# Kernel tuning notes

Hardware: AMD Instinct MI355X
Metric: run time of the kernel (lower is better)

The kernel has to match this reference:

```python
import jax, jax.numpy as jnp
import numpy as np

B, L1, L2, H = 16, 2048, 2048, 768


def setup_inputs() -> dict:
    key = jax.random.key(0)
    k1, k2, k3 = jax.random.split(key, 3)
    hi1 = jax.random.normal(k1, (B, L1, H), dtype=jnp.float32)
    hi2 = jax.random.normal(k2, (B, L2, H), dtype=jnp.float32)
    # xavier_uniform: bound = sqrt(6/(H+H))
    bound = float(np.sqrt(6.0 / (H + H)))
    wg = jax.random.uniform(k3, (H, H), dtype=jnp.float32, minval=-bound, maxval=bound)
    return {"hi1": hi1, "hi2": hi2, "wg": wg}


def reference(hi1, hi2, wg):
    # G = (hi1 @ wg) @ hi2^T  -> [B, L1, L2]
    g = jnp.einsum('bik,kl->bil', hi1, wg)
    scores = jnp.einsum('bil,bjl->bij', g, hi2)
    attn = jax.nn.softmax(scores, axis=2)
    # weighted sum over hi2 -> [B, L1, H]
    return jnp.einsum('bij,bjh->bih', attn, hi2)
```

## Files before the change

### kernel.cpp

```cpp
#include <hip/hip_runtime.h>
#include <hip/hip_bf16.h>

#define BB  16
#define LL1 2048
#define LL2 2048
#define HH  768
#define NT  24

typedef __attribute__((ext_vector_type(4))) float f32x4;
typedef __attribute__((ext_vector_type(8))) _Float16 f16x8;
typedef __attribute__((ext_vector_type(4))) _Float16 f16x4;

typedef __attribute__((address_space(3))) unsigned int lds_uint;
typedef __attribute__((address_space(1))) const unsigned int glob_uint;
__device__ __forceinline__ void gl_lds16(const void* g, void* l) {
  __builtin_amdgcn_global_load_lds((glob_uint*)g, (lds_uint*)l, 16, 0, 0);
}

__global__ __launch_bounds__(256) void k_split16(
    const float* __restrict__ in, _Float16* __restrict__ p, int n4)
{
  int i = blockIdx.x * 256 + threadIdx.x;
  int stride = gridDim.x * 256;
  for (; i < n4; i += stride) {
    f32x4 v = ((const f32x4*)in)[i];
    f16x4 o;
#pragma unroll
    for (int q = 0; q < 4; ++q) o[q] = (_Float16)v[q];
    ((f16x4*)p)[i] = o;
  }
}

__global__ __launch_bounds__(256) void k_split_wt16(
    const float* __restrict__ wg, _Float16* __restrict__ wt)
{
  __shared__ float t[32][33];
  const int k0 = blockIdx.y * 32, n0 = blockIdx.x * 32;
  const int tx = threadIdx.x & 31, ty = threadIdx.x >> 5;
#pragma unroll
  for (int r = ty; r < 32; r += 8) t[r][tx] = wg[(size_t)(k0 + r) * HH + n0 + tx];
  __syncthreads();
#pragma unroll
  for (int r = ty; r < 32; r += 8)
    wt[(size_t)(n0 + r) * HH + k0 + tx] = (_Float16)t[tx][r];
}


#define STAGE_SETUP()                                                      \
  size_t goA0, goA1, goB0; int loA0, loA1, loB0;                           \
  {                                                                        \
    int f0 = tid, f1 = 512 + tid;                                          \
    int r0 = f0 >> 2, s0 = f0 & 3, r1 = f1 >> 2, s1 = f1 & 3;              \
    goA0 = (size_t)r0 * HH + (size_t)((s0 ^ (r0 & 3)) * 8);                \
    goA1 = (size_t)r1 * HH + (size_t)((s1 ^ (r1 & 3)) * 8);                \
    loA0 = f0 * 16; loA1 = f1 * 16;                                        \
    int rb = tid >> 2, sb = tid & 3;                                       \
    goB0 = (size_t)rb * HH + (size_t)((sb ^ (rb & 3)) * 8);                \
    loB0 = tid * 16;                                                       \
  }                                                                        \
  int offA[4], offB[4];                                                    \
  _Pragma("unroll")                                                        \
  for (int mi = 0; mi < 4; ++mi) {                                         \
    int r = wm + mi * 16 + fr;                                             \
    offA[mi] = r * 64 + ((l4 * 16) ^ ((r & 3) << 4));                      \
  }                                                                        \
  _Pragma("unroll")                                                        \
  for (int ni = 0; ni < 4; ++ni) {                                         \
    int r = wn + ni * 16 + fr;                                             \
    offB[ni] = r * 64 + ((l4 * 16) ^ ((r & 3) << 4));                      \
  }

#define STG(buf, k0)                                                       \
  gl_lds16(pA + goA0 + (k0), (char*)&sA[buf][0] + loA0);                   \
  gl_lds16(pA + goA1 + (k0), (char*)&sA[buf][0] + loA1);                   \
  gl_lds16(pB + goB0 + (k0), (char*)&sB[buf][0] + loB0);

#define CMP(buf)                                                           \
  {                                                                        \
    f16x8 fa[4], fb[4];                                                    \
    _Pragma("unroll") for (int mi = 0; mi < 4; ++mi)                       \
      fa[mi] = *(const f16x8*)((const char*)&sA[buf][0] + offA[mi]);       \
    _Pragma("unroll") for (int ni = 0; ni < 4; ++ni)                       \
      fb[ni] = *(const f16x8*)((const char*)&sB[buf][0] + offB[ni]);       \
    _Pragma("unroll") for (int mi = 0; mi < 4; ++mi)                       \
      _Pragma("unroll") for (int ni = 0; ni < 4; ++ni)                     \
        acc[mi][ni] = __builtin_amdgcn_mfma_f32_16x16x32_f16(              \
            fa[mi], fb[ni], acc[mi][ni], 0, 0, 0);                         \
  }

#define KLOOP()                                                            \
  STG(0, 0);                                                               \
  asm volatile("s_waitcnt vmcnt(0)" ::: "memory");                         \
  __builtin_amdgcn_s_barrier();                                            \
  __builtin_amdgcn_sched_barrier(0);                                       \
  _Pragma("unroll")                                                        \
  for (int t = 0; t < NT; ++t) {                                           \
    if (t < NT - 1) { STG((t + 1) & 1, (t + 1) * 32); }                    \
    CMP(t & 1);                                                            \
    asm volatile("s_waitcnt vmcnt(0)" ::: "memory");                       \
    __builtin_amdgcn_s_barrier();                                          \
    __builtin_amdgcn_sched_barrier(0);                                     \
  }

__global__ __launch_bounds__(512, 4) void k_gemm_f16(
    const _Float16* __restrict__ A, const _Float16* __restrict__ Bt,
    _Float16* __restrict__ C)
{
  __shared__ _Float16 sA[2][256 * 32], sB[2][128 * 32];
  const int tid = threadIdx.x, lane = tid & 63, wave = tid >> 6;
  const int wm = (wave >> 1) * 64, wn = (wave & 1) * 64;
  const int m0 = blockIdx.y * 256, n0 = blockIdx.x * 128;
  const int fr = lane & 15, l4 = lane >> 4;
  const _Float16* pA = A  + (size_t)m0 * HH;
  const _Float16* pB = Bt + (size_t)n0 * HH;
  f32x4 acc[4][4] = {};
  STAGE_SETUP();
  KLOOP();

#pragma unroll
  for (int mi = 0; mi < 4; ++mi)
#pragma unroll
    for (int ni = 0; ni < 4; ++ni)
#pragma unroll
      for (int j = 0; j < 4; ++j) {
        int row = m0 + wm + mi * 16 + (lane >> 4) * 4 + j;
        int col = n0 + wn + ni * 16 + fr;
        C[(size_t)row * HH + col] = (_Float16)acc[mi][ni][j];
      }
}

__global__ __launch_bounds__(512, 4) void k_scores_f16(
    const _Float16* __restrict__ G, const _Float16* __restrict__ H2,
    _Float16* __restrict__ S16, float* __restrict__ Mx, int b_base)
{
  __shared__ _Float16 sA[2][256 * 32], sB[2][128 * 32];
  const int tid = threadIdx.x, lane = tid & 63, wave = tid >> 6;
  const int wm = (wave >> 1) * 64, wn = (wave & 1) * 64;
  const int z = blockIdx.z, b = b_base + z;
  const int i0 = blockIdx.y * 256, j0 = blockIdx.x * 128;
  const int fr = lane & 15, l4 = lane >> 4;
  const _Float16* pA = G  + (size_t)b * LL1 * HH + (size_t)i0 * HH;
  const _Float16* pB = H2 + (size_t)b * LL2 * HH + (size_t)j0 * HH;
  _Float16* Sp = S16 + (size_t)z * LL1 * LL2;
  float* Mp = Mx + (size_t)z * LL1 * 16;
  f32x4 acc[4][4] = {};
  STAGE_SETUP();
  KLOOP();

  __syncthreads();
  float* smax = (float*)&sA[0][0];
#pragma unroll
  for (int mi = 0; mi < 4; ++mi)
#pragma unroll
    for (int j = 0; j < 4; ++j) {
      float rm = fmaxf(fmaxf(acc[mi][0][j], acc[mi][1][j]),
                       fmaxf(acc[mi][2][j], acc[mi][3][j]));
#pragma unroll
      for (int off = 8; off >= 1; off >>= 1) rm = fmaxf(rm, __shfl_xor(rm, off));
      if ((lane & 15) == 0)
        smax[(wm + mi * 16 + (lane >> 4) * 4 + j) * 2 + (wave & 1)] = rm;
    }
  __syncthreads();

#pragma unroll
  for (int mi = 0; mi < 4; ++mi)
#pragma unroll
    for (int j = 0; j < 4; ++j) {
      int rloc = wm + mi * 16 + (lane >> 4) * 4 + j;
      float tmax = fmaxf(smax[rloc * 2], smax[rloc * 2 + 1]);
      int row = i0 + rloc;
#pragma unroll
      for (int ni = 0; ni < 4; ++ni) {
        int col = j0 + wn + ni * 16 + fr;
        float d = fmaxf(acc[mi][ni][j] - tmax, -28.0f);
        Sp[(size_t)row * LL2 + col] = (_Float16)d;
      }
    }
  if (tid < 256)
    Mp[(size_t)(i0 + tid) * 16 + (j0 >> 7)] = fmaxf(smax[tid * 2], smax[tid * 2 + 1]);
}

__global__ __launch_bounds__(512) void k_select(
    const _Float16* __restrict__ S16, const float* __restrict__ Mx,
    const _Float16* __restrict__ H2f, float* __restrict__ Out, int b_base)
{
  const int tid = threadIdx.x, lane = tid & 63, wv = tid >> 6;
  const int z = blockIdx.y, b = b_base + z;
  const int row = blockIdx.x * 4 + (wv >> 1);
  const int half = wv & 1;
  const _Float16* srow = S16 + ((size_t)z * LL1 + row) * LL2;
  const _Float16* V = H2f + (size_t)b * LL2 * HH;

  float bmax = Mx[((size_t)z * LL1 + row) * 16 + (lane & 15)];
  float m = bmax;
#pragma unroll
  for (int off = 8; off >= 1; off >>= 1) m = fmaxf(m, __shfl_xor(m, off));

  const float thr = m - 20.0f;
  float acc[6] = {};
  float lsum = 0.f;

  for (int jb = 0; jb < 16; ++jb) {
    float bj = __shfl(bmax, jb);
    if (bj <= thr) continue;
#pragma unroll
    for (int h = 0; h < 2; ++h) {
      float sval = bj + (float)srow[jb * 128 + h * 64 + lane];
      bool hit = sval > thr;
      unsigned long long mask = __ballot(hit);
      float p = hit ? __expf(sval - m) : 0.f;
      lsum += p;
      while (mask) {
        int src = __ffsll((long long)mask) - 1;
        mask &= mask - 1;
        float w = __shfl(p, src);
        int j = jb * 128 + h * 64 + src;
        const _Float16* vr = V + (size_t)j * HH + half * 384;
#pragma unroll
        for (int c = 0; c < 6; ++c) acc[c] = fmaf(w, (float)vr[lane + 64 * c], acc[c]);
      }
    }
  }
#pragma unroll
  for (int off = 32; off >= 1; off >>= 1) lsum += __shfl_xor(lsum, off);
  const float inv = 1.0f / lsum;
  float* orow = Out + ((size_t)b * LL1 + row) * HH + half * 384;
#pragma unroll
  for (int c = 0; c < 6; ++c) orow[lane + 64 * c] = acc[c] * inv;
}

extern "C" void kernel_launch(void* const* d_in, const int* in_sizes, int n_in,
                              void* d_out, int out_size, void* d_ws, size_t ws_size,
                              hipStream_t stream) {
  const float* hi1 = (const float*)d_in[0];
  const float* hi2 = (const float*)d_in[1];
  const float* wg  = (const float*)d_in[2];
  float* out = (float*)d_out;

  char* ws = (char*)d_ws;
  const size_t plane_elems = (size_t)BB * LL1 * HH;
  const size_t plane_b = plane_elems * 2;
  const size_t wt_b = (size_t)HH * HH * 2;
  const size_t s16_per_b = (size_t)LL1 * LL2 * 2;
  const size_t m_per_b = (size_t)LL1 * 16 * 4;

  _Float16* H2f = (_Float16*)ws;
  _Float16* Gf  = (_Float16*)(ws + plane_b);
  _Float16* Wtf = (_Float16*)(ws + 2 * plane_b);
  char* X = ws + 2 * plane_b + wt_b;
  _Float16* H1f = (_Float16*)X;

  const size_t fixed = 2 * plane_b + wt_b;
  int CB = 1;
  const int cand[5] = {16, 8, 4, 2, 1};
  for (int i = 0; i < 5; ++i) {
    size_t xneed = (size_t)cand[i] * (s16_per_b + m_per_b);
    if (xneed < plane_b) xneed = plane_b;
    if (fixed + xneed + 1024 <= ws_size) { CB = cand[i]; break; }
  }
  _Float16* S16 = (_Float16*)X;
  float* Mbuf = (float*)(X + (size_t)CB * s16_per_b);

  k_split16<<<4096, 256, 0, stream>>>(hi1, H1f, (int)(plane_elems / 4));
  k_split16<<<4096, 256, 0, stream>>>(hi2, H2f, (int)(plane_elems / 4));
  k_split_wt16<<<dim3(HH / 32, HH / 32), 256, 0, stream>>>(wg, Wtf);

  k_gemm_f16<<<dim3(HH / 128, (BB * LL1) / 256), 512, 0, stream>>>(H1f, Wtf, Gf);

  for (int b0 = 0; b0 < BB; b0 += CB) {
    k_scores_f16<<<dim3(LL2 / 128, LL1 / 256, CB), 512, 0, stream>>>(Gf, H2f, S16, Mbuf, b0);
    k_select<<<dim3(LL1 / 4, CB), 512, 0, stream>>>(S16, Mbuf, H2f, out, b0);
  }
}
```

Measured before the change: 400.4 us.

## Enlarge GEMM tiles to 256x256 with 64-wide K steps and split-phase prefetch

Both MFMA GEMM kernels move from 256x128 to 256x256 block tiles. Each wave now holds an 8x4 accumulator grid over a 128x64 subtile, and the K step grows to 64, split into two 32-wide LDS phases that are prefetched separately with partial vmcnt waits. The LDS swizzle changes to xor on (row>>1)&3, and s_setprio raises wave priority around the MFMA bursts. The scores kernel's row-max epilogue is adjusted to four column waves and writes two per-128-column max entries. The goal is more data reuse per LDS byte and fewer barriers per FLOP, at the cost of more registers and LDS per block and lower occupancy (launch bounds drop to 2 blocks per SM).

```diff
diff --git a/kernel.cpp b/kernel.cpp
--- a/kernel.cpp
+++ b/kernel.cpp
@@ -5,7 +5,7 @@
 #define LL1 2048
 #define LL2 2048
 #define HH  768
-#define NT  24
+#define NKT 12
 
 typedef __attribute__((ext_vector_type(4))) float f32x4;
 typedef __attribute__((ext_vector_type(8))) _Float16 f16x8;
@@ -46,138 +46,152 @@
 }
 
 
-#define STAGE_SETUP()                                                      \
-  size_t goA0, goA1, goB0; int loA0, loA1, loB0;                           \
-  {                                                                        \
-    int f0 = tid, f1 = 512 + tid;                                          \
-    int r0 = f0 >> 2, s0 = f0 & 3, r1 = f1 >> 2, s1 = f1 & 3;              \
-    goA0 = (size_t)r0 * HH + (size_t)((s0 ^ (r0 & 3)) * 8);                \
-    goA1 = (size_t)r1 * HH + (size_t)((s1 ^ (r1 & 3)) * 8);                \
-    loA0 = f0 * 16; loA1 = f1 * 16;                                        \
-    int rb = tid >> 2, sb = tid & 3;                                       \
-    goB0 = (size_t)rb * HH + (size_t)((sb ^ (rb & 3)) * 8);                \
-    loB0 = tid * 16;                                                       \
-  }                                                                        \
-  int offA[4], offB[4];                                                    \
-  _Pragma("unroll")                                                        \
-  for (int mi = 0; mi < 4; ++mi) {                                         \
-    int r = wm + mi * 16 + fr;                                             \
-    offA[mi] = r * 64 + ((l4 * 16) ^ ((r & 3) << 4));                      \
-  }                                                                        \
-  _Pragma("unroll")                                                        \
-  for (int ni = 0; ni < 4; ++ni) {                                         \
-    int r = wn + ni * 16 + fr;                                             \
-    offB[ni] = r * 64 + ((l4 * 16) ^ ((r & 3) << 4));                      \
-  }
-
-#define STG(buf, k0)                                                       \
-  gl_lds16(pA + goA0 + (k0), (char*)&sA[buf][0] + loA0);                   \
-  gl_lds16(pA + goA1 + (k0), (char*)&sA[buf][0] + loA1);                   \
-  gl_lds16(pB + goB0 + (k0), (char*)&sB[buf][0] + loB0);
-
-#define CMP(buf)                                                           \
-  {                                                                        \
-    f16x8 fa[4], fb[4];                                                    \
-    _Pragma("unroll") for (int mi = 0; mi < 4; ++mi)                       \
-      fa[mi] = *(const f16x8*)((const char*)&sA[buf][0] + offA[mi]);       \
-    _Pragma("unroll") for (int ni = 0; ni < 4; ++ni)                       \
-      fb[ni] = *(const f16x8*)((const char*)&sB[buf][0] + offB[ni]);       \
-    _Pragma("unroll") for (int mi = 0; mi < 4; ++mi)                       \
-      _Pragma("unroll") for (int ni = 0; ni < 4; ++ni)                     \
-        acc[mi][ni] = __builtin_amdgcn_mfma_f32_16x16x32_f16(              \
-            fa[mi], fb[ni], acc[mi][ni], 0, 0, 0);                         \
-  }
-
-#define KLOOP()                                                            \
-  STG(0, 0);                                                               \
-  asm volatile("s_waitcnt vmcnt(0)" ::: "memory");                         \
-  __builtin_amdgcn_s_barrier();                                            \
-  __builtin_amdgcn_sched_barrier(0);                                       \
-  _Pragma("unroll")                                                        \
-  for (int t = 0; t < NT; ++t) {                                           \
-    if (t < NT - 1) { STG((t + 1) & 1, (t + 1) * 32); }                    \
-    CMP(t & 1);                                                            \
-    asm volatile("s_waitcnt vmcnt(0)" ::: "memory");                       \
-    __builtin_amdgcn_s_barrier();                                          \
-    __builtin_amdgcn_sched_barrier(0);                                     \
-  }
-
-__global__ __launch_bounds__(512, 4) void k_gemm_f16(
+#define STAGE_SETUP()                                                       \
+  size_t gA0, gA1; int lA0, lA1;                                            \
+  {                                                                         \
+    int f0 = tid, f1 = 512 + tid;                                           \
+    int r0 = f0 >> 2, s0 = f0 & 3, r1 = f1 >> 2, s1 = f1 & 3;               \
+    gA0 = (size_t)r0 * HH + (size_t)((s0 ^ ((r0 >> 1) & 3)) * 8);           \
+    gA1 = (size_t)r1 * HH + (size_t)((s1 ^ ((r1 >> 1) & 3)) * 8);           \
+    lA0 = f0 * 16; lA1 = f1 * 16;                                           \
+  }                                                                         \
+  int offA[8], offB[4];                                                     \
+  _Pragma("unroll")                                                         \
+  for (int mi = 0; mi < 8; ++mi) {                                          \
+    int r = wml + mi * 16 + fr;                                             \
+    offA[mi] = r * 64 + ((l4 ^ ((r >> 1) & 3)) * 16);                       \
+  }                                                                         \
+  _Pragma("unroll")                                                         \
+  for (int ni = 0; ni < 4; ++ni) {                                          \
+    int r = wnl + ni * 16 + fr;                                             \
+    offB[ni] = r * 64 + ((l4 ^ ((r >> 1) & 3)) * 16);                       \
+  }
+
+#define STG_A(db, kk, kt)                                                   \
+  gl_lds16(pA + gA0 + (kt) * 64 + (kk) * 32, (char*)&sA[db][kk][0] + lA0);  \
+  gl_lds16(pA + gA1 + (kt) * 64 + (kk) * 32, (char*)&sA[db][kk][0] + lA1);
+#define STG_B(db, kk, kt)                                                   \
+  gl_lds16(pB + gA0 + (kt) * 64 + (kk) * 32, (char*)&sB[db][kk][0] + lA0);  \
+  gl_lds16(pB + gA1 + (kt) * 64 + (kk) * 32, (char*)&sB[db][kk][0] + lA1);
+
+#define PHASE(kt, kk, DOSTG, VMC)                                           \
+  {                                                                         \
+    const int cur_ = (kt) & 1;                                              \
+    f16x8 fa[8], fb[4];                                                     \
+    _Pragma("unroll") for (int mi = 0; mi < 8; ++mi)                        \
+      fa[mi] = *(const f16x8*)((const char*)&sA[cur_][kk][0] + offA[mi]);   \
+    _Pragma("unroll") for (int ni = 0; ni < 4; ++ni)                        \
+      fb[ni] = *(const f16x8*)((const char*)&sB[cur_][kk][0] + offB[ni]);   \
+    if (DOSTG) {                                                            \
+      STG_A(((kt) + 1) & 1, kk, (kt) + 1);                                  \
+      STG_B(((kt) + 1) & 1, kk, (kt) + 1);                                  \
+    }                                                                       \
+    __builtin_amdgcn_s_setprio(1);                                          \
+    _Pragma("unroll") for (int mi = 0; mi < 8; ++mi)                        \
+      _Pragma("unroll") for (int ni = 0; ni < 4; ++ni)                      \
+        acc[mi][ni] = __builtin_amdgcn_mfma_f32_16x16x32_f16(               \
+            fa[mi], fb[ni], acc[mi][ni], 0, 0, 0);                          \
+    __builtin_amdgcn_s_setprio(0);                                          \
+    asm volatile("s_waitcnt vmcnt(" VMC ")" ::: "memory");                  \
+    __builtin_amdgcn_s_barrier();                                           \
+    __builtin_amdgcn_sched_barrier(0);                                      \
+  }
+
+#define KLOOP()                                                             \
+  STG_A(0, 0, 0); STG_B(0, 0, 0);                                           \
+  STG_A(0, 1, 0); STG_B(0, 1, 0);                                           \
+  asm volatile("s_waitcnt vmcnt(4)" ::: "memory");                          \
+  __builtin_amdgcn_s_barrier();                                             \
+  __builtin_amdgcn_sched_barrier(0);                                        \
+  _Pragma("unroll")                                                         \
+  for (int t = 0; t < NKT - 1; ++t) {                                       \
+    PHASE(t, 0, 1, "4");                                                    \
+    PHASE(t, 1, 1, "4");                                                    \
+  }                                                                         \
+  PHASE(NKT - 1, 0, 0, "0");                                                \
+  PHASE(NKT - 1, 1, 0, "0");
+
+__global__ __launch_bounds__(512, 2) void k_gemm_f16(
     const _Float16* __restrict__ A, const _Float16* __restrict__ Bt,
     _Float16* __restrict__ C)
 {
-  __shared__ _Float16 sA[2][256 * 32], sB[2][128 * 32];
+  __shared__ _Float16 sA[2][2][8192], sB[2][2][8192];
   const int tid = threadIdx.x, lane = tid & 63, wave = tid >> 6;
-  const int wm = (wave >> 1) * 64, wn = (wave & 1) * 64;
-  const int m0 = blockIdx.y * 256, n0 = blockIdx.x * 128;
+  const int wml = (wave >> 2) * 128, wnl = (wave & 3) * 64;
+  const int m0 = blockIdx.y * 256, n0 = blockIdx.x * 256;
   const int fr = lane & 15, l4 = lane >> 4;
   const _Float16* pA = A  + (size_t)m0 * HH;
   const _Float16* pB = Bt + (size_t)n0 * HH;
-  f32x4 acc[4][4] = {};
+  f32x4 acc[8][4] = {};
   STAGE_SETUP();
   KLOOP();
 
 #pragma unroll
-  for (int mi = 0; mi < 4; ++mi)
+  for (int mi = 0; mi < 8; ++mi)
 #pragma unroll
     for (int ni = 0; ni < 4; ++ni)
 #pragma unroll
       for (int j = 0; j < 4; ++j) {
-        int row = m0 + wm + mi * 16 + (lane >> 4) * 4 + j;
-        int col = n0 + wn + ni * 16 + fr;
+        int row = m0 + wml + mi * 16 + l4 * 4 + j;
+        int col = n0 + wnl + ni * 16 + fr;
         C[(size_t)row * HH + col] = (_Float16)acc[mi][ni][j];
       }
 }
 
-__global__ __launch_bounds__(512, 4) void k_scores_f16(
+__global__ __launch_bounds__(512, 2) void k_scores_f16(
     const _Float16* __restrict__ G, const _Float16* __restrict__ H2,
     _Float16* __restrict__ S16, float* __restrict__ Mx, int b_base)
 {
-  __shared__ _Float16 sA[2][256 * 32], sB[2][128 * 32];
+  __shared__ _Float16 sA[2][2][8192], sB[2][2][8192];
   const int tid = threadIdx.x, lane = tid & 63, wave = tid >> 6;
-  const int wm = (wave >> 1) * 64, wn = (wave & 1) * 64;
+  const int wml = (wave >> 2) * 128, wnl = (wave & 3) * 64;
   const int z = blockIdx.z, b = b_base + z;
-  const int i0 = blockIdx.y * 256, j0 = blockIdx.x * 128;
+  const int i0 = blockIdx.y * 256, j0 = blockIdx.x * 256;
   const int fr = lane & 15, l4 = lane >> 4;
   const _Float16* pA = G  + (size_t)b * LL1 * HH + (size_t)i0 * HH;
   const _Float16* pB = H2 + (size_t)b * LL2 * HH + (size_t)j0 * HH;
   _Float16* Sp = S16 + (size_t)z * LL1 * LL2;
   float* Mp = Mx + (size_t)z * LL1 * 16;
-  f32x4 acc[4][4] = {};
+  f32x4 acc[8][4] = {};
   STAGE_SETUP();
   KLOOP();
 
   __syncthreads();
-  float* smax = (float*)&sA[0][0];
-#pragma unroll
-  for (int mi = 0; mi < 4; ++mi)
+  float* smax = (float*)&sA[0][0][0];
+#pragma unroll
+  for (int mi = 0; mi < 8; ++mi)
 #pragma unroll
     for (int j = 0; j < 4; ++j) {
       float rm = fmaxf(fmaxf(acc[mi][0][j], acc[mi][1][j]),
                        fmaxf(acc[mi][2][j], acc[mi][3][j]));
 #pragma unroll
       for (int off = 8; off >= 1; off >>= 1) rm = fmaxf(rm, __shfl_xor(rm, off));
-      if ((lane & 15) == 0)
-        smax[(wm + mi * 16 + (lane >> 4) * 4 + j) * 2 + (wave & 1)] = rm;
+      if (fr == 0)
+        smax[(wml + mi * 16 + l4 * 4 + j) * 4 + (wave & 3)] = rm;
     }
   __syncthreads();
 
-#pragma unroll
-  for (int mi = 0; mi < 4; ++mi)
+  const int hb = (wave & 3) >> 1;
+#pragma unroll
+  for (int mi = 0; mi < 8; ++mi)
 #pragma unroll
     for (int j = 0; j < 4; ++j) {
-      int rloc = wm + mi * 16 + (lane >> 4) * 4 + j;
-      float tmax = fmaxf(smax[rloc * 2], smax[rloc * 2 + 1]);
+      int rloc = wml + mi * 16 + l4 * 4 + j;
+      float tmax = fmaxf(smax[rloc * 4 + 2 * hb], smax[rloc * 4 + 2 * hb + 1]);
       int row = i0 + rloc;
 #pragma unroll
       for (int ni = 0; ni < 4; ++ni) {
-        int col = j0 + wn + ni * 16 + fr;
+        int col = j0 + wnl + ni * 16 + fr;
         float d = fmaxf(acc[mi][ni][j] - tmax, -28.0f);
         Sp[(size_t)row * LL2 + col] = (_Float16)d;
       }
     }
-  if (tid < 256)
-    Mp[(size_t)(i0 + tid) * 16 + (j0 >> 7)] = fmaxf(smax[tid * 2], smax[tid * 2 + 1]);
+  if (tid < 256) {
+    float m0v = fmaxf(smax[tid * 4 + 0], smax[tid * 4 + 1]);
+    float m1v = fmaxf(smax[tid * 4 + 2], smax[tid * 4 + 3]);
+    Mp[(size_t)(i0 + tid) * 16 + (j0 >> 7)]     = m0v;
+    Mp[(size_t)(i0 + tid) * 16 + (j0 >> 7) + 1] = m1v;
+  }
 }
 
 __global__ __launch_bounds__(512) void k_select(
@@ -265,10 +279,10 @@
   k_split16<<<4096, 256, 0, stream>>>(hi2, H2f, (int)(plane_elems / 4));
   k_split_wt16<<<dim3(HH / 32, HH / 32), 256, 0, stream>>>(wg, Wtf);
 
-  k_gemm_f16<<<dim3(HH / 128, (BB * LL1) / 256), 512, 0, stream>>>(H1f, Wtf, Gf);
+  k_gemm_f16<<<dim3(HH / 256, (BB * LL1) / 256), 512, 0, stream>>>(H1f, Wtf, Gf);
 
   for (int b0 = 0; b0 < BB; b0 += CB) {
-    k_scores_f16<<<dim3(LL2 / 128, LL1 / 256, CB), 512, 0, stream>>>(Gf, H2f, S16, Mbuf, b0);
+    k_scores_f16<<<dim3(LL2 / 256, LL1 / 256, CB), 512, 0, stream>>>(Gf, H2f, S16, Mbuf, b0);
     k_select<<<dim3(LL1 / 4, CB), 512, 0, stream>>>(S16, Mbuf, H2f, out, b0);
   }
 }
```

Result: no change. 398.2 us (-0.5%).
